# Performance work log

Measured on AMD Instinct MI355X. Metric: run time of the kernel, lower is better.

Reference implementation:

```python
import jax, jax.numpy as jnp
import numpy as np

# Sizes: batch=32, in_channels=32, out_channels=64, grid 256x256, modes1=modes2=32
B, CI, CO, NX, NY, M1, M2 = 32, 32, 64, 256, 256, 32, 32


def setup_inputs() -> dict:
    key = jax.random.key(0)
    k1, k2, k3 = jax.random.split(key, 3)
    scale = 1.0 / (CI * CO)
    return {
        "x": jax.random.normal(k1, (B, CI, NX, NY), dtype=jnp.float32),
        "w_real": scale * jax.random.uniform(k2, (CI, CO, 2 * M1, M2 + 1), dtype=jnp.float32),
        "w_imag": scale * jax.random.uniform(k3, (CI, CO, 2 * M1, M2 + 1), dtype=jnp.float32),
        "modes1": M1,
        "modes2": M2,
    }


def reference(x, w_real, w_imag, modes1, modes2):
    # rfft2 with 'forward' normalization (divide by nx*ny), as in torch.fft.rfft2(norm='forward')
    xf = jnp.fft.rfft2(x, norm="forward")  # (b, i, nx, ny//2+1) complex64
    # resize_rfft2(xf, (2*modes1, 2*modes2)) in the truncation regime (nx >= 2*m1, ny//2+1 >= m2+1):
    # keep first modes2+1 columns (rfft axis) and the first/last modes1 rows (full fft axis).
    xt = jnp.concatenate(
        [xf[..., :modes1, : modes2 + 1], xf[..., -modes1:, : modes2 + 1]], axis=-2
    )  # (b, i, 2*m1, m2+1)
    W = w_real + 1j * w_imag  # (i, o, 2*m1, m2+1) complex
    # complex channel mixing, keep only real part
    y = jnp.einsum("bixy,ioxy->boxy", xt, W).real  # (b, o, 2*m1, m2+1)
    # signed mode-sum: double-count conjugate-symmetric modes, correct the (0,0) DC mode
    out = (
        2.0 * jnp.sum(y[..., :modes1, :], axis=(-2, -1))
        + 2.0 * jnp.sum(y[..., modes1:, 1:], axis=(-2, -1))
        - y[..., 0, 0]
    )  # (b, o)
    return out
```

## Files before the change

kernel.cpp:

```cpp
#include <hip/hip_runtime.h>
#include <hip/hip_bf16.h>
#include <math.h>

#define BATCH 32
#define CIn   32
#define COut  64

typedef __attribute__((ext_vector_type(8))) short bf16x8;
typedef __attribute__((ext_vector_type(4))) float f32x4;

#define OB_T1F  0u
#define OB_ECF  40960u
#define OB_ESF  73728u
#define OB_XTB  106496u
#define OB_PART 8757248u

__device__ __forceinline__ ushort f2bf(float f) {
    union { float f; uint u; } v; v.f = f;
    uint r = (v.u + 0x7FFFu + ((v.u >> 16) & 1u)) >> 16;
    return (ushort)r;
}

__device__ __forceinline__ bf16x8 cvt8(f32x4 lo, f32x4 hi) {
    union { __hip_bfloat162 h2[4]; bf16x8 v; } u;
    u.h2[0] = __float22bfloat162_rn(make_float2(lo[0], lo[1]));
    u.h2[1] = __float22bfloat162_rn(make_float2(lo[2], lo[3]));
    u.h2[2] = __float22bfloat162_rn(make_float2(hi[0], hi[1]));
    u.h2[3] = __float22bfloat162_rn(make_float2(hi[2], hi[3]));
    return u.v;
}
__device__ __forceinline__ ushort f2bfn(float f) {
    union { __hip_bfloat16 h; ushort u; } v;
    v.h = __float2bfloat16(f);
    return v.u;
}

#define NB0 0
#define NB1 16
#define NB2 32
#define NB3 48
#define NB4 50

__global__ void fno_tw(ushort* __restrict__ T1f, ushort* __restrict__ Ecf,
                       ushort* __restrict__ Esf) {
    const int nb[5] = {NB0, NB1, NB2, NB3, NB4};
    int idx = blockIdx.x * 256 + threadIdx.x;
    const float w0 = 6.28318530717958647692f / 256.0f;
    if (idx < 20480) {
        int i = idx & 7, l = (idx >> 3) & 63, ct = idx >> 9;
        int c = ct / 5, t = ct - 5 * c;
        int k = 32 * c + 8 * (l >> 4) + i;
        int n = nb[t] + (l & 15);
        int ky = n >> 1, s = n & 1;
        int m = (k * ky) & 255;
        float v = s ? -sinf(w0 * (float)m) : cosf(w0 * (float)m);
        T1f[idx] = f2bf(v * (1.0f / 65536.0f));
    }
    if (idx < 16384) {
        int i = idx & 7, l = (idx >> 3) & 63, km = idx >> 9;
        int ks = km >> 2, mt = km & 3;
        int xx = ks * 32 + ((l >> 4) << 3) + i;
        int kx = mt * 16 + (l & 15);
        int kxa = (kx < 32) ? kx : kx + 192;
        int m = (xx * kxa) & 255;
        Ecf[idx] = f2bf(cosf(w0 * (float)m));
        Esf[idx] = f2bf(-sinf(w0 * (float)m));
    }
}

#define STAGE_S(S) do {                                                            \
    int s_ = (S);                                                                  \
    float* lb_ = &smx[s_ & 1][0];                                                  \
    const float* gb_ = x + ((size_t)p * 256 + s_ * 16) * 256;                      \
    _Pragma("unroll")                                                              \
    for (int jj = 0; jj < 4; ++jj) {                                               \
        int rl_ = w * 4 + jj;                                                      \
        int sg_ = lane ^ (rl_ & 7);             \
        const float* gp_ = gb_ + (size_t)rl_ * 256 + (sg_ << 2);                   \
        char* lp_ = (char*)lb_ + (rl_ << 10);                                      \
        __builtin_amdgcn_global_load_lds(                                          \
            (const __attribute__((address_space(1))) unsigned int*)gp_,            \
            (__attribute__((address_space(3))) unsigned int*)lp_, 16, 0, 0);       \
    } } while (0)

#define WAITV(N) do {                                                              \
    asm volatile("s_waitcnt vmcnt(" #N ")" ::: "memory");                          \
    __builtin_amdgcn_sched_barrier(0); } while (0)

#define BAR do {                                                                   \
    __builtin_amdgcn_s_barrier();                                                  \
    __builtin_amdgcn_sched_barrier(0); } while (0)

__global__ __launch_bounds__(256, 2)
void fno_fused(const float* __restrict__ x, const ushort* __restrict__ T1f,
               const ushort* __restrict__ Ecf, const ushort* __restrict__ Esf,
               ushort* __restrict__ XTb) {
    __shared__ __align__(16) float smx[2][4096];
    __shared__ __align__(16) ushort Yt[16896];
    const int nb[5] = {NB0, NB1, NB2, NB3, NB4};
    const int tid  = threadIdx.x;
    const int lane = tid & 63;
    const int w    = tid >> 6;
    const int r0   = lane & 15;
    const int g    = lane >> 4;
    const int xr   = r0 & 7;
    const int p    = blockIdx.x;

    bf16x8 bfr0[8], bfr4[8];
    const bf16x8* bp = (const bf16x8*)T1f;
#pragma unroll
    for (int c = 0; c < 8; ++c) bfr0[c] = bp[(c * 5 + w) * 64 + lane];
    if (w == 3) {
#pragma unroll
        for (int c = 0; c < 8; ++c) bfr4[c] = bp[(c * 5 + 4) * 64 + lane];
    }

    STAGE_S(0); STAGE_S(1);
    WAITV(4);
    BAR;

    for (int s = 0; s < 16; ++s) {
        f32x4 a0 = {0, 0, 0, 0}, a4 = {0, 0, 0, 0};
        const char* rowb = (const char*)&smx[s & 1][0] + (r0 << 10);
#pragma unroll
        for (int c = 0; c < 8; ++c) {
            f32x4 lo = *(const f32x4*)(rowb + ((((c << 3) + (g << 1)    ) ^ xr) << 4));
            f32x4 hi = *(const f32x4*)(rowb + ((((c << 3) + (g << 1) + 1) ^ xr) << 4));
            bf16x8 a = cvt8(lo, hi);
            a0 = __builtin_amdgcn_mfma_f32_16x16x32_bf16(a, bfr0[c], a0, 0, 0, 0);
            if (w == 3)
                a4 = __builtin_amdgcn_mfma_f32_16x16x32_bf16(a, bfr4[c], a4, 0, 0, 0);
        }
        {
            int xr0 = (s << 4) + (g << 2);
            int n0  = nb[w] + r0;
            int us0 = n0 * 256 + ((((xr0 >> 3) ^ (n0 & 31)) << 3) | (xr0 & 7));
            union { __hip_bfloat162 h[2]; uint2 u; } uu;
            uu.h[0] = __float22bfloat162_rn(make_float2(a0[0], a0[1]));
            uu.h[1] = __float22bfloat162_rn(make_float2(a0[2], a0[3]));
            *(uint2*)&Yt[us0] = uu.u;
            if (w == 3 && r0 >= 14) {
                int n4  = 50 + r0;
                int us4 = n4 * 256 + ((((xr0 >> 3) ^ (n4 & 31)) << 3) | (xr0 & 7));
                union { __hip_bfloat162 h[2]; uint2 u; } vv;
                vv.h[0] = __float22bfloat162_rn(make_float2(a4[0], a4[1]));
                vv.h[1] = __float22bfloat162_rn(make_float2(a4[2], a4[3]));
                *(uint2*)&Yt[us4] = vv.u;
            }
        }
        BAR;
        if (s + 2 < 16) {
            STAGE_S(s + 2);
            WAITV(4);
        } else {
            WAITV(0);
        }
        BAR;
    }
    __syncthreads();

    const int mt = w;
    f32x4 P1[5], P2[5];
#pragma unroll
    for (int t = 0; t < 5; ++t) { P1[t] = (f32x4){0,0,0,0}; P2[t] = (f32x4){0,0,0,0}; }

    const bf16x8* ecp = (const bf16x8*)Ecf;
    const bf16x8* esp = (const bf16x8*)Esf;
#pragma unroll
    for (int ks = 0; ks < 8; ++ks) {
        bf16x8 ea = ecp[(ks * 4 + mt) * 64 + lane];
        bf16x8 es = esp[(ks * 4 + mt) * 64 + lane];
#pragma unroll
        for (int t = 0; t < 5; ++t) {
            int n = nb[t] + r0;
            bf16x8 b = *(const bf16x8*)&Yt[n * 256 + ((((ks << 2) + g) ^ (n & 31)) << 3)];
            P1[t] = __builtin_amdgcn_mfma_f32_16x16x32_bf16(ea, b, P1[t], 0, 0, 0);
            P2[t] = __builtin_amdgcn_mfma_f32_16x16x32_bf16(es, b, P2[t], 0, 0, 0);
        }
    }

    ushort* xtl = (ushort*)&smx[0][0];
#pragma unroll
    for (int t = 0; t < 5; ++t) {
        int n  = nb[t] + r0;
        int ky = n >> 1, im = n & 1;
#pragma unroll
        for (int j = 0; j < 4; ++j) {
            float v2x = __shfl_xor(P2[t][j], 1);
            if (t == 4 && r0 < 14) continue;
            int kx = mt * 16 + 4 * g + j;
            float val = im ? (P1[t][j] + v2x) : (P1[t][j] - v2x);
            float wgt = (kx < 32) ? ((kx == 0 && ky == 0) ? 1.f : 2.f)
                                  : ((ky == 0) ? 0.f : 2.f);
            if (im) wgt = -wgt;
            xtl[kx * 66 + n] = f2bfn(wgt * val);
        }
    }
    __syncthreads();

    const uint4* srcq = (const uint4*)xtl;
    uint4* dstq = (uint4*)(XTb + (size_t)p * 4224);
    for (int e = tid; e < 528; e += 256) dstq[e] = srcq[e];
}

__global__ __launch_bounds__(256)
void fno_gemm3(const ushort* __restrict__ XTb, const float* __restrict__ Wr,
               const float* __restrict__ Wi, float* __restrict__ part) {
    const int blk = blockIdx.x;
    const int ic  = blk / 22;
    const int sc  = blk - ic * 22;
    const int tid = threadIdx.x;
    const int lane = tid & 63;
    const int w    = tid >> 6;
    const int r0   = lane & 15;
    const int g    = lane >> 4;
    const int o    = (w << 4) + r0;

    const float* wrp = Wr + ((size_t)ic * 64 + o) * 2112 + sc * 96 + 4 * g;
    const float* wip = Wi + ((size_t)ic * 64 + o) * 2112 + sc * 96 + 4 * g;
    const ushort* a0 = XTb + ((size_t)r0 * 32 + ic) * 4224 + sc * 192 + 8 * g;
    const ushort* a1 = a0 + (size_t)16 * 32 * 4224;

    f32x4 acc0 = {0,0,0,0}, acc1 = {0,0,0,0};
#pragma unroll
    for (int st = 0; st < 6; ++st) {
        f32x4 vr = *(const f32x4*)(wrp + st * 16);
        f32x4 vi = *(const f32x4*)(wip + st * 16);
        union { __hip_bfloat162 h2[4]; bf16x8 v; } ub;
        ub.h2[0] = __float22bfloat162_rn(make_float2(vr[0], vi[0]));
        ub.h2[1] = __float22bfloat162_rn(make_float2(vr[1], vi[1]));
        ub.h2[2] = __float22bfloat162_rn(make_float2(vr[2], vi[2]));
        ub.h2[3] = __float22bfloat162_rn(make_float2(vr[3], vi[3]));
        bf16x8 af0 = *(const bf16x8*)(a0 + st * 32);
        bf16x8 af1 = *(const bf16x8*)(a1 + st * 32);
        acc0 = __builtin_amdgcn_mfma_f32_16x16x32_bf16(af0, ub.v, acc0, 0, 0, 0);
        acc1 = __builtin_amdgcn_mfma_f32_16x16x32_bf16(af1, ub.v, acc1, 0, 0, 0);
    }

    float* pp = part + (size_t)blk * 2048;
#pragma unroll
    for (int j = 0; j < 4; ++j) {
        pp[(4 * g + j) * 64 + o]      = acc0[j];
        pp[(16 + 4 * g + j) * 64 + o] = acc1[j];
    }
}

__global__ __launch_bounds__(256)
void fno_reduce(const float* __restrict__ part, float* __restrict__ out) {
    __shared__ float red[256];
    const int tid = threadIdx.x;
    const int il  = tid & 7;
    const int js  = tid >> 3;
    const int idx = blockIdx.x * 8 + il;

    float s = 0.f;
#pragma unroll
    for (int t = 0; t < 22; ++t)
        s += part[(size_t)(js + 32 * t) * 2048 + idx];
    red[tid] = s;
    __syncthreads();

    if (tid < 8) {
        float v = 0.f;
#pragma unroll
        for (int q = 0; q < 32; ++q) v += red[q * 8 + tid];
        out[blockIdx.x * 8 + tid] = v;
    }
}

extern "C" void kernel_launch(void* const* d_in, const int* in_sizes, int n_in,
                              void* d_out, int out_size, void* d_ws, size_t ws_size,
                              hipStream_t stream) {
    const float* x  = (const float*)d_in[0];
    const float* wr = (const float*)d_in[1];
    const float* wi = (const float*)d_in[2];
    float* out = (float*)d_out;
    char* ws   = (char*)d_ws;

    ushort* T1f = (ushort*)(ws + OB_T1F);
    ushort* Ecf = (ushort*)(ws + OB_ECF);
    ushort* Esf = (ushort*)(ws + OB_ESF);
    ushort* XTb = (ushort*)(ws + OB_XTB);
    float* part = (float*)(ws + OB_PART);

    fno_tw<<<80, 256, 0, stream>>>(T1f, Ecf, Esf);
    fno_fused<<<1024, 256, 0, stream>>>(x, T1f, Ecf, Esf, XTb);
    fno_gemm3<<<704, 256, 0, stream>>>(XTb, wr, wi, part);
    fno_reduce<<<256, 256, 0, stream>>>(part, out);
}
```

Baseline: 80.55 us.

## Process two planes per block with cross-plane prefetch and register-held twiddles

```diff
diff --git a/kernel.cpp b/kernel.cpp
--- a/kernel.cpp
+++ b/kernel.cpp
@@ -68,10 +68,10 @@
     }
 }
 
-#define STAGE_S(S) do {                                                            \
+#define STAGE_S(P, S) do {                                                         \
     int s_ = (S);                                                                  \
     float* lb_ = &smx[s_ & 1][0];                                                  \
-    const float* gb_ = x + ((size_t)p * 256 + s_ * 16) * 256;                      \
+    const float* gb_ = x + ((size_t)(P) * 256 + s_ * 16) * 256;                    \
     _Pragma("unroll")                                                              \
     for (int jj = 0; jj < 4; ++jj) {                                               \
         int rl_ = w * 4 + jj;                                                      \
@@ -87,6 +87,10 @@
     asm volatile("s_waitcnt vmcnt(" #N ")" ::: "memory");                          \
     __builtin_amdgcn_sched_barrier(0); } while (0)
 
+#define WAITL0 do {                                                                \
+    asm volatile("s_waitcnt lgkmcnt(0)" ::: "memory");                             \
+    __builtin_amdgcn_sched_barrier(0); } while (0)
+
 #define BAR do {                                                                   \
     __builtin_amdgcn_s_barrier();                                                  \
     __builtin_amdgcn_sched_barrier(0); } while (0)
@@ -97,6 +101,7 @@
                ushort* __restrict__ XTb) {
     __shared__ __align__(16) float smx[2][4096];
     __shared__ __align__(16) ushort Yt[16896];
+    __shared__ __align__(16) ushort xtls[4224];
     const int nb[5] = {NB0, NB1, NB2, NB3, NB4};
     const int tid  = threadIdx.x;
     const int lane = tid & 63;
@@ -104,103 +109,130 @@
     const int r0   = lane & 15;
     const int g    = lane >> 4;
     const int xr   = r0 & 7;
-    const int p    = blockIdx.x;
-
+    const int blk  = blockIdx.x;
+
+    bf16x8 ecr[8], esr[8];
+    {
+        const bf16x8* ecp = (const bf16x8*)Ecf;
+        const bf16x8* esp = (const bf16x8*)Esf;
+#pragma unroll
+        for (int ks = 0; ks < 8; ++ks) {
+            ecr[ks] = ecp[(ks * 4 + w) * 64 + lane];
+            esr[ks] = esp[(ks * 4 + w) * 64 + lane];
+        }
+    }
     bf16x8 bfr0[8], bfr4[8];
-    const bf16x8* bp = (const bf16x8*)T1f;
-#pragma unroll
-    for (int c = 0; c < 8; ++c) bfr0[c] = bp[(c * 5 + w) * 64 + lane];
-    if (w == 3) {
-#pragma unroll
-        for (int c = 0; c < 8; ++c) bfr4[c] = bp[(c * 5 + 4) * 64 + lane];
-    }
-
-    STAGE_S(0); STAGE_S(1);
-    WAITV(4);
-    BAR;
-
-    for (int s = 0; s < 16; ++s) {
-        f32x4 a0 = {0, 0, 0, 0}, a4 = {0, 0, 0, 0};
-        const char* rowb = (const char*)&smx[s & 1][0] + (r0 << 10);
-#pragma unroll
-        for (int c = 0; c < 8; ++c) {
-            f32x4 lo = *(const f32x4*)(rowb + ((((c << 3) + (g << 1)    ) ^ xr) << 4));
-            f32x4 hi = *(const f32x4*)(rowb + ((((c << 3) + (g << 1) + 1) ^ xr) << 4));
-            bf16x8 a = cvt8(lo, hi);
-            a0 = __builtin_amdgcn_mfma_f32_16x16x32_bf16(a, bfr0[c], a0, 0, 0, 0);
-            if (w == 3)
-                a4 = __builtin_amdgcn_mfma_f32_16x16x32_bf16(a, bfr4[c], a4, 0, 0, 0);
-        }
+    {
+        const bf16x8* bp = (const bf16x8*)T1f;
+#pragma unroll
+        for (int c = 0; c < 8; ++c) bfr0[c] = bp[(c * 5 + w) * 64 + lane];
+        if (w == 3) {
+#pragma unroll
+            for (int c = 0; c < 8; ++c) bfr4[c] = bp[(c * 5 + 4) * 64 + lane];
+        }
+    }
+    WAITV(0);
+
+    for (int pl = 0; pl < 2; ++pl) {
+        const int p = blk * 2 + pl;
+
+        if (pl == 0) {
+            STAGE_S(p, 0); STAGE_S(p, 1);
+            WAITV(4);
+            BAR;
+        }
+
+        for (int s = 0; s < 16; ++s) {
+            f32x4 a0 = {0, 0, 0, 0}, a4 = {0, 0, 0, 0};
+            const char* rowb = (const char*)&smx[s & 1][0] + (r0 << 10);
+#pragma unroll
+            for (int c = 0; c < 8; ++c) {
+                f32x4 lo = *(const f32x4*)(rowb + ((((c << 3) + (g << 1)    ) ^ xr) << 4));
+                f32x4 hi = *(const f32x4*)(rowb + ((((c << 3) + (g << 1) + 1) ^ xr) << 4));
+                bf16x8 a = cvt8(lo, hi);
+                a0 = __builtin_amdgcn_mfma_f32_16x16x32_bf16(a, bfr0[c], a0, 0, 0, 0);
+                if (w == 3)
+                    a4 = __builtin_amdgcn_mfma_f32_16x16x32_bf16(a, bfr4[c], a4, 0, 0, 0);
+            }
+            {
+                int xr0 = (s << 4) + (g << 2);
+                int n0  = nb[w] + r0;
+                int us0 = n0 * 256 + ((((xr0 >> 3) ^ (n0 & 31)) << 3) | (xr0 & 7));
+                union { __hip_bfloat162 h[2]; uint2 u; } uu;
+                uu.h[0] = __float22bfloat162_rn(make_float2(a0[0], a0[1]));
+                uu.h[1] = __float22bfloat162_rn(make_float2(a0[2], a0[3]));
+                *(uint2*)&Yt[us0] = uu.u;
+                if (w == 3 && r0 >= 14) {
+                    int n4  = 50 + r0;
+                    int us4 = n4 * 256 + ((((xr0 >> 3) ^ (n4 & 31)) << 3) | (xr0 & 7));
+                    union { __hip_bfloat162 h[2]; uint2 u; } vv;
+                    vv.h[0] = __float22bfloat162_rn(make_float2(a4[0], a4[1]));
+                    vv.h[1] = __float22bfloat162_rn(make_float2(a4[2], a4[3]));
+                    *(uint2*)&Yt[us4] = vv.u;
+                }
+            }
+            WAITL0;
+            BAR;
+            if (s <= 13) {
+                STAGE_S(p, s + 2);
+                WAITV(4);
+                BAR;
+            } else if (s == 14) {
+                if (pl == 0) {
+                    STAGE_S(p + 1, 0);
+                    WAITV(4);
+                } else {
+                    WAITV(0);
+                }
+                BAR;
+            } else {
+                if (pl == 0) STAGE_S(p + 1, 1);
+            }
+        }
+
+        f32x4 P1[5], P2[5];
+#pragma unroll
+        for (int t = 0; t < 5; ++t) { P1[t] = (f32x4){0,0,0,0}; P2[t] = (f32x4){0,0,0,0}; }
+
+#pragma unroll
+        for (int ks = 0; ks < 8; ++ks) {
+#pragma unroll
+            for (int t = 0; t < 5; ++t) {
+                int n = nb[t] + r0;
+                bf16x8 b = *(const bf16x8*)&Yt[n * 256 + ((((ks << 2) + g) ^ (n & 31)) << 3)];
+                P1[t] = __builtin_amdgcn_mfma_f32_16x16x32_bf16(ecr[ks], b, P1[t], 0, 0, 0);
+                P2[t] = __builtin_amdgcn_mfma_f32_16x16x32_bf16(esr[ks], b, P2[t], 0, 0, 0);
+            }
+        }
+
+#pragma unroll
+        for (int t = 0; t < 5; ++t) {
+            int n  = nb[t] + r0;
+            int ky = n >> 1, im = n & 1;
+#pragma unroll
+            for (int j = 0; j < 4; ++j) {
+                float v2x = __shfl_xor(P2[t][j], 1);
+                if (t == 4 && r0 < 14) continue;
+                int kx = w * 16 + 4 * g + j;
+                float val = im ? (P1[t][j] + v2x) : (P1[t][j] - v2x);
+                float wgt = (kx < 32) ? ((kx == 0 && ky == 0) ? 1.f : 2.f)
+                                      : ((ky == 0) ? 0.f : 2.f);
+                if (im) wgt = -wgt;
+                xtls[kx * 66 + n] = f2bfn(wgt * val);
+            }
+        }
+        WAITL0;
+        BAR;
         {
-            int xr0 = (s << 4) + (g << 2);
-            int n0  = nb[w] + r0;
-            int us0 = n0 * 256 + ((((xr0 >> 3) ^ (n0 & 31)) << 3) | (xr0 & 7));
-            union { __hip_bfloat162 h[2]; uint2 u; } uu;
-            uu.h[0] = __float22bfloat162_rn(make_float2(a0[0], a0[1]));
-            uu.h[1] = __float22bfloat162_rn(make_float2(a0[2], a0[3]));
-            *(uint2*)&Yt[us0] = uu.u;
-            if (w == 3 && r0 >= 14) {
-                int n4  = 50 + r0;
-                int us4 = n4 * 256 + ((((xr0 >> 3) ^ (n4 & 31)) << 3) | (xr0 & 7));
-                union { __hip_bfloat162 h[2]; uint2 u; } vv;
-                vv.h[0] = __float22bfloat162_rn(make_float2(a4[0], a4[1]));
-                vv.h[1] = __float22bfloat162_rn(make_float2(a4[2], a4[3]));
-                *(uint2*)&Yt[us4] = vv.u;
-            }
-        }
-        BAR;
-        if (s + 2 < 16) {
-            STAGE_S(s + 2);
-            WAITV(4);
-        } else {
+            const uint4* srcq = (const uint4*)xtls;
+            uint4* dstq = (uint4*)(XTb + (size_t)p * 4224);
+            for (int e = tid; e < 528; e += 256) dstq[e] = srcq[e];
+        }
+        if (pl == 0) {
             WAITV(0);
-        }
-        BAR;
-    }
-    __syncthreads();
-
-    const int mt = w;
-    f32x4 P1[5], P2[5];
-#pragma unroll
-    for (int t = 0; t < 5; ++t) { P1[t] = (f32x4){0,0,0,0}; P2[t] = (f32x4){0,0,0,0}; }
-
-    const bf16x8* ecp = (const bf16x8*)Ecf;
-    const bf16x8* esp = (const bf16x8*)Esf;
-#pragma unroll
-    for (int ks = 0; ks < 8; ++ks) {
-        bf16x8 ea = ecp[(ks * 4 + mt) * 64 + lane];
-        bf16x8 es = esp[(ks * 4 + mt) * 64 + lane];
-#pragma unroll
-        for (int t = 0; t < 5; ++t) {
-            int n = nb[t] + r0;
-            bf16x8 b = *(const bf16x8*)&Yt[n * 256 + ((((ks << 2) + g) ^ (n & 31)) << 3)];
-            P1[t] = __builtin_amdgcn_mfma_f32_16x16x32_bf16(ea, b, P1[t], 0, 0, 0);
-            P2[t] = __builtin_amdgcn_mfma_f32_16x16x32_bf16(es, b, P2[t], 0, 0, 0);
-        }
-    }
-
-    ushort* xtl = (ushort*)&smx[0][0];
-#pragma unroll
-    for (int t = 0; t < 5; ++t) {
-        int n  = nb[t] + r0;
-        int ky = n >> 1, im = n & 1;
-#pragma unroll
-        for (int j = 0; j < 4; ++j) {
-            float v2x = __shfl_xor(P2[t][j], 1);
-            if (t == 4 && r0 < 14) continue;
-            int kx = mt * 16 + 4 * g + j;
-            float val = im ? (P1[t][j] + v2x) : (P1[t][j] - v2x);
-            float wgt = (kx < 32) ? ((kx == 0 && ky == 0) ? 1.f : 2.f)
-                                  : ((ky == 0) ? 0.f : 2.f);
-            if (im) wgt = -wgt;
-            xtl[kx * 66 + n] = f2bfn(wgt * val);
-        }
-    }
-    __syncthreads();
-
-    const uint4* srcq = (const uint4*)xtl;
-    uint4* dstq = (uint4*)(XTb + (size_t)p * 4224);
-    for (int e = tid; e < 528; e += 256) dstq[e] = srcq[e];
+            BAR;
+        }
+    }
 }
 
 __global__ __launch_bounds__(256)
@@ -284,7 +316,7 @@
     float* part = (float*)(ws + OB_PART);
 
     fno_tw<<<80, 256, 0, stream>>>(T1f, Ecf, Esf);
-    fno_fused<<<1024, 256, 0, stream>>>(x, T1f, Ecf, Esf, XTb);
+    fno_fused<<<512, 256, 0, stream>>>(x, T1f, Ecf, Esf, XTb);
     fno_gemm3<<<704, 256, 0, stream>>>(XTb, wr, wi, part);
     fno_reduce<<<256, 256, 0, stream>>>(part, out);
 }
```

Result: slower. 100.7 us (+25.0%).
